# Kernel optimization log

Measured on AMD Instinct MI355X. Metric: run time of the kernel, lower is better.

## Reference

```python
import jax, jax.numpy as jnp
import numpy as np

N_QUBITS = 10
LAYERS = 4


def _ry(theta):
    c = jnp.cos(theta / 2).astype(jnp.complex64)
    s = jnp.sin(theta / 2).astype(jnp.complex64)
    return jnp.array([[c, -s], [s, c]], dtype=jnp.complex64)


def _rot(phi, theta, omega):
    # Rot = RZ(omega) RY(theta) RZ(phi)  (PennyLane convention)
    c = jnp.cos(theta / 2)
    s = jnp.sin(theta / 2)
    e_mm = jnp.exp(-0.5j * (phi + omega))
    e_pm = jnp.exp(0.5j * (phi - omega))
    e_mp = jnp.exp(-0.5j * (phi - omega))
    e_pp = jnp.exp(0.5j * (phi + omega))
    return jnp.array([[e_mm * c, -e_pm * s], [e_mp * s, e_pp * c]], dtype=jnp.complex64)


def _apply_1q(state, U, q):
    # state: (2,)*n complex; contract qubit axis q with 2x2 gate
    s = jnp.tensordot(U, state, axes=[[1], [q]])
    return jnp.moveaxis(s, 0, q)


def _apply_cnot(state, c, t):
    s = jnp.moveaxis(state, (c, t), (0, 1))
    s = jnp.stack([s[0], s[1, ::-1]], axis=0)
    return jnp.moveaxis(s, (0, 1), (c, t))


def _circuit(angles, weights):
    # angles: (n_qubits,) float32, weights: (layers, n_qubits, 3) float32
    n = N_QUBITS
    state = jnp.zeros((2 ** n,), dtype=jnp.complex64).at[0].set(1.0).reshape((2,) * n)
    for q in range(n):  # RY angle embedding
        state = _apply_1q(state, _ry(angles[q]), q)
    for l in range(LAYERS):  # strongly-entangling layers
        for q in range(n):
            state = _apply_1q(state, _rot(weights[l, q, 0], weights[l, q, 1], weights[l, q, 2]), q)
        for q in range(n):  # CNOT ring
            state = _apply_cnot(state, q, (q + 1) % n)
    probs = state.real ** 2 + state.imag ** 2  # (2,)*n
    zexp = []
    for q in range(n):
        p = probs.sum(axis=tuple(a for a in range(n) if a != q))
        zexp.append(p[0] - p[1])
    return jnp.stack(zexp)  # (n_qubits,)


def setup_inputs() -> dict:
    key = jax.random.key(0)
    ks = jax.random.split(key, 6)
    B, D = 8192, 784
    return {
        "x": jax.random.normal(ks[0], (B, D), dtype=jnp.float32),
        "Wp": jax.random.normal(ks[1], (N_QUBITS, D), dtype=jnp.float32) * (1.0 / np.sqrt(D)),
        "bp": jax.random.normal(ks[2], (N_QUBITS,), dtype=jnp.float32) * 0.01,
        "q_weights": jax.random.normal(ks[3], (LAYERS, N_QUBITS, 3), dtype=jnp.float32) * 0.01,
        "Wo": jax.random.normal(ks[4], (10, N_QUBITS), dtype=jnp.float32) * (1.0 / np.sqrt(N_QUBITS)),
        "bo": jax.random.normal(ks[5], (10,), dtype=jnp.float32) * 0.01,
    }


def reference(x, Wp, bp, q_weights, Wo, bo):
    # input projection + tanh
    h = jnp.tanh(x @ Wp.T + bp)  # (B, n_qubits)
    # batched quantum circuit (vmapped statevector simulation)
    q_out = jax.vmap(_circuit, in_axes=(0, None))(h, q_weights)  # (B, n_qubits)
    return q_out @ Wo.T + bo  # (B, 10) logits
```

## Files before the change

### kernel.cpp

```cpp
#include <hip/hip_runtime.h>

#define NQ      10
#define NLAYERS 4
#define D_IN    784
#define BLOCK   256


typedef __attribute__((ext_vector_type(2))) float f2;

__device__ __forceinline__ f2 sp(float v) { f2 r; r.x = v; r.y = v; return r; }
__device__ __forceinline__ f2 swapc(f2 v) { return __builtin_shufflevector(v, v, 1, 0); }

template<int LB>
__device__ __forceinline__ float lx(float v) {
    if constexpr (LB == 1) {
        return __int_as_float(__builtin_amdgcn_update_dpp(
            0, __float_as_int(v), 0xB1, 0xF, 0xF, false));
    } else if constexpr (LB == 2) {
        return __int_as_float(__builtin_amdgcn_update_dpp(
            0, __float_as_int(v), 0x4E, 0xF, 0xF, false));
    } else if constexpr (LB == 8) {
        return __int_as_float(__builtin_amdgcn_update_dpp(
            0, __float_as_int(v), 0x128, 0xF, 0xF, false));
    } else {
        return __shfl_xor(v, LB, 64);
    }
}

template<int LB>
__device__ __forceinline__ f2 lx2(f2 v) {
    f2 r; r.x = lx<LB>(v.x); r.y = lx<LB>(v.y); return r;
}

template<int HALF>
__device__ __forceinline__ void plswap(f2 &d, f2 &s) {
    if constexpr (HALF == 32) {
        auto rx = __builtin_amdgcn_permlane32_swap(__float_as_int(d.x), __float_as_int(s.x), false, false);
        auto ry = __builtin_amdgcn_permlane32_swap(__float_as_int(d.y), __float_as_int(s.y), false, false);
        d.x = __int_as_float(rx[0]); s.x = __int_as_float(rx[1]);
        d.y = __int_as_float(ry[0]); s.y = __int_as_float(ry[1]);
    } else {
        auto rx = __builtin_amdgcn_permlane16_swap(__float_as_int(d.x), __float_as_int(s.x), false, false);
        auto ry = __builtin_amdgcn_permlane16_swap(__float_as_int(d.y), __float_as_int(s.y), false, false);
        d.x = __int_as_float(rx[0]); s.x = __int_as_float(rx[1]);
        d.y = __int_as_float(ry[0]); s.y = __int_as_float(ry[1]);
    }
}

template<int HALF>
__device__ __forceinline__ void ry_pl(f2 (&re)[8], f2 (&im)[8], float c, float s) {
#pragma unroll
    for (int a = 0; a < 8; a += 2) {
        f2 ur = re[a], vr = re[a + 1], ui = im[a], vi = im[a + 1];
        plswap<HALF>(ur, vr); plswap<HALF>(ui, vi);
        f2 nur = sp(c)*ur - sp(s)*vr;   f2 nui = sp(c)*ui - sp(s)*vi;
        f2 nvr = sp(s)*ur + sp(c)*vr;   f2 nvi = sp(s)*ui + sp(c)*vi;
        plswap<HALF>(nur, nvr); plswap<HALF>(nui, nvi);
        re[a] = nur; re[a + 1] = nvr; im[a] = nui; im[a + 1] = nvi;
    }
}

__device__ __forceinline__ void ry0_fused(f2 (&re)[8], f2 (&im)[8], float c, float s) {
    f2 K1, K2, K3, K4;
    K1.x =  c; K1.y = -s;   K2.x = -s; K2.y =  c;
    K3.x =  s; K3.y =  c;   K4.x =  c; K4.y =  s;
#pragma unroll
    for (int a = 0; a < 8; a += 2) {
        f2 ur = re[a], vr = re[a + 1], ui = im[a], vi = im[a + 1];
        plswap<32>(ur, vr); plswap<32>(ui, vi);
        f2 nur = K1*ur + K2*vr;   f2 nui = K1*ui + K2*vi;
        f2 nvr = K3*ur + K4*vr;   f2 nvi = K3*ui + K4*vi;
        plswap<32>(nur, nvr); plswap<32>(nui, nvi);
        re[a] = nur; re[a + 1] = nvr; im[a] = nui; im[a + 1] = nvi;
    }
}

template<int LB>
__device__ __forceinline__ void ry_lane(f2 (&re)[8], f2 (&im)[8], int lane, float c, float s) {
    const float o = (lane & LB) ? s : -s;
#pragma unroll
    for (int a = 0; a < 8; a++) {
        f2 ore = lx2<LB>(re[a]);
        f2 oim = lx2<LB>(im[a]);
        re[a] = sp(c)*re[a] + sp(o)*ore;
        im[a] = sp(c)*im[a] + sp(o)*oim;
    }
}

template<int MB>
__device__ __forceinline__ void ry_reg(f2 (&re)[8], f2 (&im)[8], float c, float s) {
#pragma unroll
    for (int a = 0; a < 8; a++) {
        if (!(a & MB)) {
            const int a1 = a | MB;
            f2 r0 = re[a], r1 = re[a1], i0 = im[a], i1 = im[a1];
            re[a]  = sp(c)*r0 - sp(s)*r1;   re[a1] = sp(s)*r0 + sp(c)*r1;
            im[a]  = sp(c)*i0 - sp(s)*i1;   im[a1] = sp(s)*i0 + sp(c)*i1;
        }
    }
}

__device__ __forceinline__ void ry_comp(f2 (&re)[8], f2 (&im)[8], float c, float s) {
    f2 Ks; Ks.x = -s; Ks.y = s;
#pragma unroll
    for (int a = 0; a < 8; a++) {
        f2 sre = swapc(re[a]), sim = swapc(im[a]);
        re[a] = sp(c)*re[a] + Ks*sre;
        im[a] = sp(c)*im[a] + Ks*sim;
    }
}

template<bool XOR0>
__device__ __forceinline__ void diag_apply(f2 (&re)[8], f2 (&im)[8], int lane,
                                           const float* lz, const f2* DC, const f2* DS) {
    float lp = 0.f;
    lp += (lane & 16) ? lz[1] : -lz[1];
    lp += (lane &  8) ? lz[2] : -lz[2];
    lp += (lane &  4) ? lz[3] : -lz[3];
    lp += (lane &  2) ? lz[4] : -lz[4];
    lp += (lane &  1) ? lz[5] : -lz[5];
    const float t0 = (lane & 32) ? lz[0] : -lz[0];
    f2 cl, sl;
    if constexpr (XOR0) {
        float sa, ca, sb, cb;
        sincosf(lp + t0, &sa, &ca);
        sincosf(lp - t0, &sb, &cb);
        cl.x = ca; cl.y = cb; sl.x = sa; sl.y = sb;
    } else {
        float sa, ca;
        sincosf(lp + t0, &sa, &ca);
        cl = sp(ca); sl = sp(sa);
    }
#pragma unroll
    for (int a = 0; a < 8; a++) {
        f2 cr = cl*DC[a] - sl*DS[a];
        f2 ci = cl*DS[a] + sl*DC[a];
        f2 nr = cr*re[a] - ci*im[a];
        f2 ni = cr*im[a] + ci*re[a];
        re[a] = nr; im[a] = ni;
    }
}

__device__ __forceinline__ void swapf2(f2 &a, f2 &b) { f2 t = a; a = b; b = t; }

__device__ __forceinline__ void ring(f2 (&re)[8], f2 (&im)[8], int lane, int bidx) {
#pragma unroll
    for (int a = 0; a < 8; a++) {
        re[a].x = __int_as_float(__builtin_amdgcn_ds_bpermute(bidx, __float_as_int(re[a].x)));
        re[a].y = __int_as_float(__builtin_amdgcn_ds_bpermute(bidx, __float_as_int(re[a].y)));
        im[a].x = __int_as_float(__builtin_amdgcn_ds_bpermute(bidx, __float_as_int(im[a].x)));
        im[a].y = __int_as_float(__builtin_amdgcn_ds_bpermute(bidx, __float_as_int(im[a].y)));
    }
    const bool ctl = (lane & 1) != 0;
#pragma unroll
    for (int a = 0; a < 4; a++) {
        f2 A0 = re[a], A1 = re[a + 4], B0 = im[a], B1 = im[a + 4];
        f2 n0, n1, m0, m1;
        n0.x = ctl ? A1.x : A0.x;  n0.y = ctl ? A1.y : A0.y;
        n1.x = ctl ? A0.x : A1.x;  n1.y = ctl ? A0.y : A1.y;
        m0.x = ctl ? B1.x : B0.x;  m0.y = ctl ? B1.y : B0.y;
        m1.x = ctl ? B0.x : B1.x;  m1.y = ctl ? B0.y : B1.y;
        re[a] = n0; re[a + 4] = n1; im[a] = m0; im[a + 4] = m1;
    }
    swapf2(re[4], re[6]); swapf2(re[5], re[7]); swapf2(im[4], im[6]); swapf2(im[5], im[7]);
    swapf2(re[2], re[3]); swapf2(re[6], re[7]); swapf2(im[2], im[3]); swapf2(im[6], im[7]);
#pragma unroll
    for (int a = 1; a < 8; a += 2) { re[a] = swapc(re[a]); im[a] = swapc(im[a]); }
}

__global__ __launch_bounds__(BLOCK)
__attribute__((amdgpu_waves_per_eu(2, 8)))
void qnet_kernel(
    const float* __restrict__ x,
    const float* __restrict__ Wp,
    const float* __restrict__ bp,
    const float* __restrict__ qw,
    const float* __restrict__ Wo,
    const float* __restrict__ bo,
    float* __restrict__ out, int B)
{
    __shared__ float ryt[NLAYERS * NQ * 2];
    __shared__ float lzt[NLAYERS * 2 * 6];
    __shared__ __align__(8) f2 dct[NLAYERS * 2 * 8];
    __shared__ __align__(8) f2 dst[NLAYERS * 2 * 8];

    const int tid  = threadIdx.x;
    const int lane = tid & 63;
    const int s    = blockIdx.x * (BLOCK / 64) + (tid >> 6);

    if (tid < NLAYERS * NQ) {
        const int l = tid / NQ, q = tid % NQ;
        float th = qw[tid * 3 + 1];
        float sc, cc; sincosf(0.5f * th, &sc, &cc);
        ryt[tid * 2] = cc; ryt[tid * 2 + 1] = sc;
        if (q < 6) {
            lzt[(l * 2 + 0) * 6 + q] = 0.5f * qw[tid * 3 + 0];
            lzt[(l * 2 + 1) * 6 + q] = 0.5f * qw[tid * 3 + 2];
        }
    }
    if (tid >= 64 && tid < 128) {
        const int idx = tid - 64;
        const int l = idx >> 4, t = (idx >> 3) & 1, a = idx & 7;
        const float* ql = qw + (size_t)l * NQ * 3;
        const int off = t ? 2 : 0;
        const float p6 = 0.5f * ql[6 * 3 + off], p7 = 0.5f * ql[7 * 3 + off];
        const float p8 = 0.5f * ql[8 * 3 + off], p9 = 0.5f * ql[9 * 3 + off];
        const float base = ((a & 4) ? p6 : -p6) + ((a & 2) ? p7 : -p7) + ((a & 1) ? p8 : -p8);
        float s0, c0, s1, c1;
        sincosf(base - p9, &s0, &c0);
        sincosf(base + p9, &s1, &c1);
        f2 dc; dc.x = c0; dc.y = c1;
        f2 ds; ds.x = s0; ds.y = s1;
        dct[(l * 2 + t) * 8 + a] = dc;
        dst[(l * 2 + t) * 8 + a] = ds;
    }
    __syncthreads();
    if (s >= B) return;

    float acc[NQ];
#pragma unroll
    for (int q = 0; q < NQ; q++) acc[q] = 0.f;
    const float* xr = x + (size_t)s * D_IN;
#pragma unroll
    for (int it = 0; it < 3; it++) {
        const int d = (it * 64 + lane) * 4;
        float4 xv = *(const float4*)(xr + d);
#pragma unroll
        for (int q = 0; q < NQ; q++) {
            float4 wv = *(const float4*)(Wp + q * D_IN + d);
            acc[q] += xv.x * wv.x + xv.y * wv.y + xv.z * wv.z + xv.w * wv.w;
        }
    }
    if (lane < 4) {
        const int d = (192 + lane) * 4;
        float4 xv = *(const float4*)(xr + d);
#pragma unroll
        for (int q = 0; q < NQ; q++) {
            float4 wv = *(const float4*)(Wp + q * D_IN + d);
            acc[q] += xv.x * wv.x + xv.y * wv.y + xv.z * wv.z + xv.w * wv.w;
        }
    }
#pragma unroll
    for (int q = 0; q < NQ; q++) {
#pragma unroll
        for (int o = 1; o < 64; o <<= 1) acc[q] += __shfl_xor(acc[q], o, 64);
    }
    float myc = 1.f, mys = 0.f;
    if (lane < NQ) {
        float h = tanhf(acc[lane] + bp[lane]);
        sincosf(0.5f * h, &mys, &myc);
    }

    f2 re[8], im[8];
    float lf = 1.f;
    {
        float cq, sq;
#define SEL(Q, MASK) cq = __shfl(myc, Q, 64); sq = __shfl(mys, Q, 64); \
                     lf *= (lane & MASK) ? sq : cq;
        SEL(0, 32) SEL(1, 16) SEL(2, 8) SEL(3, 4) SEL(4, 2) SEL(5, 1)
#undef SEL
        const float c6 = __shfl(myc, 6, 64), s6 = __shfl(mys, 6, 64);
        const float c7 = __shfl(myc, 7, 64), s7 = __shfl(mys, 7, 64);
        const float c8 = __shfl(myc, 8, 64), s8 = __shfl(mys, 8, 64);
        const float c9 = __shfl(myc, 9, 64), s9 = __shfl(mys, 9, 64);
#pragma unroll
        for (int a = 0; a < 8; a++) {
            float t = ((a & 4) ? s6 : c6) * ((a & 2) ? s7 : c7) * ((a & 1) ? s8 : c8) * lf;
            re[a].x = t * c9; re[a].y = t * s9;
            im[a] = sp(0.f);
        }
    }

    const int bidx = (lane ^ (lane >> 1)) << 2;

    {
        const float* rl = ryt;
        diag_apply<false>(re, im, lane, lzt, dct, dst);
        ry_pl<32>(re, im, rl[0], rl[1]);
        ry_pl<16>(re, im, rl[2], rl[3]);
        ry_lane<8>(re, im, lane, rl[4], rl[5]);
        ry_lane<4>(re, im, lane, rl[6], rl[7]);
        ry_lane<2>(re, im, lane, rl[8], rl[9]);
        ry_lane<1>(re, im, lane, rl[10], rl[11]);
        ry_reg<4>(re, im, rl[12], rl[13]);
        ry_reg<2>(re, im, rl[14], rl[15]);
        ry_reg<1>(re, im, rl[16], rl[17]);
        ry_comp(re, im, rl[18], rl[19]);
        diag_apply<false>(re, im, lane, lzt + 6, dct + 8, dst + 8);
        ring(re, im, lane, bidx);
    }

    for (int l = 1; l < NLAYERS; l++) {
        const float* rl = ryt + l * NQ * 2;
        diag_apply<true>(re, im, lane, lzt + (l * 2) * 6,
                         dct + (l * 2) * 8, dst + (l * 2) * 8);
        ry0_fused(re, im, rl[0], rl[1]);
        ry_pl<16>(re, im, rl[2], rl[3]);
        ry_lane<8>(re, im, lane, rl[4], rl[5]);
        ry_lane<4>(re, im, lane, rl[6], rl[7]);
        ry_lane<2>(re, im, lane, rl[8], rl[9]);
        ry_lane<1>(re, im, lane, rl[10], rl[11]);
        ry_reg<4>(re, im, rl[12], rl[13]);
        ry_reg<2>(re, im, rl[14], rl[15]);
        ry_reg<1>(re, im, rl[16], rl[17]);
        ry_comp(re, im, rl[18], rl[19]);
        if (l < NLAYERS - 1)
            diag_apply<false>(re, im, lane, lzt + (l * 2 + 1) * 6,
                              dct + (l * 2 + 1) * 8, dst + (l * 2 + 1) * 8);
        ring(re, im, lane, bidx);
    }

    f2 S2 = {0.f, 0.f}, z62 = {0.f, 0.f}, z72 = {0.f, 0.f}, z82 = {0.f, 0.f};
#pragma unroll
    for (int a = 0; a < 8; a++) {
        f2 p = re[a] * re[a] + im[a] * im[a];
        S2 += p;
        if (a & 4) z62 -= p; else z62 += p;
        if (a & 2) z72 -= p; else z72 += p;
        if (a & 1) z82 -= p; else z82 += p;
    }
    const float Ssum = S2.x + S2.y;
    const float Sdif = S2.x - S2.y;
    float zq[NQ];
    zq[0] = (lane & 32) ? -Sdif : Sdif;
    zq[1] = (lane & 16) ? -Ssum : Ssum;
    zq[2] = (lane &  8) ? -Ssum : Ssum;
    zq[3] = (lane &  4) ? -Ssum : Ssum;
    zq[4] = (lane &  2) ? -Ssum : Ssum;
    zq[5] = (lane &  1) ? -Ssum : Ssum;
    zq[6] = z62.x + z62.y;
    zq[7] = z72.x + z72.y;
    zq[8] = z82.x + z82.y;
    zq[9] = Sdif;
#pragma unroll
    for (int q = 0; q < NQ; q++) {
#pragma unroll
        for (int o = 1; o < 64; o <<= 1) zq[q] += __shfl_xor(zq[q], o, 64);
    }

    if (lane < NQ) {
        const float* wrow = Wo + lane * NQ;
        float o0 = bo[lane];
#pragma unroll
        for (int q = 0; q < NQ; q++) o0 += zq[q] * wrow[q];
        out[(size_t)s * NQ + lane] = o0;
    }
}

extern "C" void kernel_launch(void* const* d_in, const int* in_sizes, int n_in,
                              void* d_out, int out_size, void* d_ws, size_t ws_size,
                              hipStream_t stream) {
    const float* x  = (const float*)d_in[0];
    const float* Wp = (const float*)d_in[1];
    const float* bp = (const float*)d_in[2];
    const float* qw = (const float*)d_in[3];
    const float* Wo = (const float*)d_in[4];
    const float* bo = (const float*)d_in[5];
    float* out = (float*)d_out;

    const int B = in_sizes[0] / D_IN;
    const int spb = BLOCK / 64;
    const int blocks = (B + spb - 1) / spb;
    hipLaunchKernelGGL(qnet_kernel, dim3(blocks), dim3(BLOCK), 0, stream,
                       x, Wp, bp, qw, Wo, bo, out, B);
}
```

Measured before the change: 139.6 us.

## Fold RZ phases across CNOT ring into precomputed per-lane diagonal tables

Drops the per-thread sincosf phase computation in each diagonal step. Each layer's trailing RZ(omega) diagonal is merged, through the CNOT ring permutation, with the next layer's leading RZ(phi) diagonal, giving one diagonal instead of two per layer boundary. Per-lane phase factors and per-register factors indexed by lane parity are precomputed once per block into shared memory. In exchange the block prologue does more setup work and the tables depend on getting the parity bookkeeping exactly right.

```diff
diff --git a/kernel.cpp b/kernel.cpp
--- a/kernel.cpp
+++ b/kernel.cpp
@@ -110,27 +110,9 @@
     }
 }
 
-template<bool XOR0>
-__device__ __forceinline__ void diag_apply(f2 (&re)[8], f2 (&im)[8], int lane,
-                                           const float* lz, const f2* DC, const f2* DS) {
-    float lp = 0.f;
-    lp += (lane & 16) ? lz[1] : -lz[1];
-    lp += (lane &  8) ? lz[2] : -lz[2];
-    lp += (lane &  4) ? lz[3] : -lz[3];
-    lp += (lane &  2) ? lz[4] : -lz[4];
-    lp += (lane &  1) ? lz[5] : -lz[5];
-    const float t0 = (lane & 32) ? lz[0] : -lz[0];
-    f2 cl, sl;
-    if constexpr (XOR0) {
-        float sa, ca, sb, cb;
-        sincosf(lp + t0, &sa, &ca);
-        sincosf(lp - t0, &sb, &cb);
-        cl.x = ca; cl.y = cb; sl.x = sa; sl.y = sb;
-    } else {
-        float sa, ca;
-        sincosf(lp + t0, &sa, &ca);
-        cl = sp(ca); sl = sp(sa);
-    }
+__device__ __forceinline__ void diag_tbl(f2 (&re)[8], f2 (&im)[8], f2 lp,
+                                         const f2* DC, const f2* DS) {
+    f2 cl = sp(lp.x), sl = sp(lp.y);
 #pragma unroll
     for (int a = 0; a < 8; a++) {
         f2 cr = cl*DC[a] - sl*DS[a];
@@ -180,39 +162,89 @@
     float* __restrict__ out, int B)
 {
     __shared__ float ryt[NLAYERS * NQ * 2];
-    __shared__ float lzt[NLAYERS * 2 * 6];
-    __shared__ __align__(8) f2 dct[NLAYERS * 2 * 8];
-    __shared__ __align__(8) f2 dst[NLAYERS * 2 * 8];
+    __shared__ __align__(8) f2 lt[4][64];
+    __shared__ __align__(8) f2 vtc[3][4][8];
+    __shared__ __align__(8) f2 vts[3][4][8];
+    __shared__ __align__(8) f2 dc0[8], ds0[8];
 
     const int tid  = threadIdx.x;
     const int lane = tid & 63;
     const int s    = blockIdx.x * (BLOCK / 64) + (tid >> 6);
 
     if (tid < NLAYERS * NQ) {
-        const int l = tid / NQ, q = tid % NQ;
         float th = qw[tid * 3 + 1];
         float sc, cc; sincosf(0.5f * th, &sc, &cc);
         ryt[tid * 2] = cc; ryt[tid * 2 + 1] = sc;
-        if (q < 6) {
-            lzt[(l * 2 + 0) * 6 + q] = 0.5f * qw[tid * 3 + 0];
-            lzt[(l * 2 + 1) * 6 + q] = 0.5f * qw[tid * 3 + 2];
-        }
-    }
-    if (tid >= 64 && tid < 128) {
-        const int idx = tid - 64;
-        const int l = idx >> 4, t = (idx >> 3) & 1, a = idx & 7;
-        const float* ql = qw + (size_t)l * NQ * 3;
-        const int off = t ? 2 : 0;
-        const float p6 = 0.5f * ql[6 * 3 + off], p7 = 0.5f * ql[7 * 3 + off];
-        const float p8 = 0.5f * ql[8 * 3 + off], p9 = 0.5f * ql[9 * 3 + off];
-        const float base = ((a & 4) ? p6 : -p6) + ((a & 2) ? p7 : -p7) + ((a & 1) ? p8 : -p8);
+    }
+    {
+        const int tbl = tid >> 6, ln = tid & 63;
+        float ph = 0.f;
+        if (tbl == 0) {
+#pragma unroll
+            for (int q = 0; q < 6; q++) {
+                float a = 0.5f * qw[q * 3 + 0];
+                ph += ((ln >> (5 - q)) & 1) ? a : -a;
+            }
+        } else {
+            const float* qwW = qw + (size_t)(tbl - 1) * NQ * 3;
+            const float* qwP = qw + (size_t)tbl * NQ * 3;
+            int par = 0;
+#pragma unroll
+            for (int q = 0; q < 6; q++) {
+                int v = (ln >> (5 - q)) & 1;
+                float wa = 0.5f * qwW[q * 3 + 2];
+                ph += v ? wa : -wa;
+                par ^= v;
+                if (q >= 1) {
+                    float pa = 0.5f * qwP[q * 3 + 0];
+                    ph += par ? pa : -pa;
+                }
+            }
+        }
+        float sn, cs; sincosf(ph, &sn, &cs);
+        f2 e; e.x = cs; e.y = sn;
+        lt[tbl][ln] = e;
+    }
+    if (tid < 96) {
+        const int b = tid >> 5, rem = tid & 31, p = rem >> 3, a = rem & 7;
+        const int pL = p >> 1, pL1 = p & 1;
+        const int v6 = (a >> 2) & 1, v7 = (a >> 1) & 1, v8 = a & 1;
+        const float* qwW = qw + (size_t)b * NQ * 3;
+        const float* qwP = qw + (size_t)(b + 1) * NQ * 3;
+        const float w6 = 0.5f * qwW[6 * 3 + 2], w7 = 0.5f * qwW[7 * 3 + 2];
+        const float w8 = 0.5f * qwW[8 * 3 + 2], w9 = 0.5f * qwW[9 * 3 + 2];
+        const float p0 = 0.5f * qwP[0 * 3 + 0], p6 = 0.5f * qwP[6 * 3 + 0];
+        const float p7 = 0.5f * qwP[7 * 3 + 0], p8 = 0.5f * qwP[8 * 3 + 0];
+        const float p9 = 0.5f * qwP[9 * 3 + 0];
+        const float base = (v6 ? w6 : -w6) + (v7 ? w7 : -w7) + (v8 ? w8 : -w8);
+        const int h7 = v6 ^ v7, h8 = h7 ^ v8;
+        const float sL  = pL  ? -1.f : 1.f;
+        const float sL1 = pL1 ? -1.f : 1.f;
+        const float t1b = (v6 ? p6 : -p6) + (h7 ? p7 : -p7) + (h8 ? p8 : -p8);
+        float cC[2], sC[2];
+#pragma unroll
+        for (int C = 0; C < 2; C++) {
+            float ph = base + (C ? w9 : -w9)
+                     + sL  * (t1b + ((h8 ^ C) ? p9 : -p9))
+                     + sL1 * ((h8 ^ C) ? p0 : -p0);
+            sincosf(ph, &sC[C], &cC[C]);
+        }
+        f2 ec; ec.x = cC[0]; ec.y = cC[1];
+        f2 es; es.x = sC[0]; es.y = sC[1];
+        vtc[b][p][a] = ec; vts[b][p][a] = es;
+    }
+    if (tid < 8) {
+        const int a = tid;
+        const int v6 = (a >> 2) & 1, v7 = (a >> 1) & 1, v8 = a & 1;
+        const float p6 = 0.5f * qw[6 * 3 + 0], p7 = 0.5f * qw[7 * 3 + 0];
+        const float p8 = 0.5f * qw[8 * 3 + 0], p9 = 0.5f * qw[9 * 3 + 0];
+        const float base = (v6 ? p6 : -p6) + (v7 ? p7 : -p7) + (v8 ? p8 : -p8);
         float s0, c0, s1, c1;
         sincosf(base - p9, &s0, &c0);
         sincosf(base + p9, &s1, &c1);
         f2 dc; dc.x = c0; dc.y = c1;
         f2 ds; ds.x = s0; ds.y = s1;
-        dct[(l * 2 + t) * 8 + a] = dc;
-        dst[(l * 2 + t) * 8 + a] = ds;
+        dc0[a] = dc; ds0[a] = ds;
     }
     __syncthreads();
     if (s >= B) return;
@@ -272,10 +304,11 @@
     }
 
     const int bidx = (lane ^ (lane >> 1)) << 2;
+    const int pvar = ((__popc(lane) & 1) << 1) | (__popc(lane & 31) & 1);
 
     {
         const float* rl = ryt;
-        diag_apply<false>(re, im, lane, lzt, dct, dst);
+        diag_tbl(re, im, lt[0][lane], dc0, ds0);
         ry_pl<32>(re, im, rl[0], rl[1]);
         ry_pl<16>(re, im, rl[2], rl[3]);
         ry_lane<8>(re, im, lane, rl[4], rl[5]);
@@ -286,14 +319,12 @@
         ry_reg<2>(re, im, rl[14], rl[15]);
         ry_reg<1>(re, im, rl[16], rl[17]);
         ry_comp(re, im, rl[18], rl[19]);
-        diag_apply<false>(re, im, lane, lzt + 6, dct + 8, dst + 8);
+        diag_tbl(re, im, lt[1][lane], vtc[0][pvar], vts[0][pvar]);
         ring(re, im, lane, bidx);
     }
 
     for (int l = 1; l < NLAYERS; l++) {
         const float* rl = ryt + l * NQ * 2;
-        diag_apply<true>(re, im, lane, lzt + (l * 2) * 6,
-                         dct + (l * 2) * 8, dst + (l * 2) * 8);
         ry0_fused(re, im, rl[0], rl[1]);
         ry_pl<16>(re, im, rl[2], rl[3]);
         ry_lane<8>(re, im, lane, rl[4], rl[5]);
@@ -305,8 +336,7 @@
         ry_reg<1>(re, im, rl[16], rl[17]);
         ry_comp(re, im, rl[18], rl[19]);
         if (l < NLAYERS - 1)
-            diag_apply<false>(re, im, lane, lzt + (l * 2 + 1) * 6,
-                              dct + (l * 2 + 1) * 8, dst + (l * 2 + 1) * 8);
+            diag_tbl(re, im, lt[l + 1][lane], vtc[l][pvar], vts[l][pvar]);
         ring(re, im, lane, bidx);
     }
 
```

After: 135.6 us, median of 2. 1.03x faster.
